# Performance work log

Measured on AMD Instinct MI355X. Metric: run time of the kernel, lower is better.

## Reference

```python
import jax, jax.numpy as jnp
import numpy as np

DIM = 512      # projection dimension
NCOLS = 16384  # number of vectors being projected


def _gram_schmidt(w):
    """Modified Gram-Schmidt, column by column, faithful to the torch loop.

    Columns of q beyond the current index are zero, so the inner loop can
    safely run over all `dim` columns (projections onto zero columns are
    no-ops), which keeps the body shape-static for lax.fori_loop.
    """
    dim = w.shape[1]
    q = jnp.zeros_like(w).at[:, 0].set(w[:, 0] / jnp.linalg.norm(w[:, 0]))

    def outer(i, q):
        v = w[:, i]
        def inner(j, v):
            # modified GS: v is updated sequentially against each prior q_j
            return v - jnp.dot(v, q[:, j]) * q[:, j]
        v = jax.lax.fori_loop(0, dim, inner, v)
        return q.at[:, i].set(v / jnp.linalg.norm(v))

    return jax.lax.fori_loop(1, dim, outer, q)


def setup_inputs() -> dict:
    key = jax.random.key(0)
    k1, k2, k3 = jax.random.split(key, 3)
    return {
        "x": jax.random.normal(k1, (DIM, NCOLS), dtype=jnp.float32),
        "weight": jax.random.normal(k2, (DIM, DIM), dtype=jnp.float32),   # OrthogonalMatrix.weight ~ randn
        "D_param": jax.random.uniform(k3, (DIM,), dtype=jnp.float32),     # ProjectionNetwork.D ~ rand
    }


def reference(x, weight, D_param):
    U = _gram_schmidt(weight)                 # (dim, dim) orthogonal
    D = jax.nn.sigmoid(D_param)               # (dim,)
    P = (U * D[None, :]) @ U.T                # U @ diag(D) @ U^T
    return P @ x                              # (dim, ncols)
```

## Files before the change

### kernel.cpp

```cpp
#include <hip/hip_runtime.h>
#include <hip/hip_bf16.h>

#define DIM 512
#define NCOLS 16384

typedef __bf16 bf16x8 __attribute__((ext_vector_type(8)));
typedef float f32x4 __attribute__((ext_vector_type(4)));

__device__ __forceinline__ unsigned short f2bf(float f) {
  unsigned u = __builtin_bit_cast(unsigned, f);
  u += 0x7FFFu + ((u >> 16) & 1u);
  return (unsigned short)(u >> 16);
}

__global__ __launch_bounds__(256) void k_gram(const float* __restrict__ W,
                                              double* __restrict__ G) {
  __shared__ float Wa[16][34];
  __shared__ float Wb[16][34];
  const int t = threadIdx.x;
  const int tx = t & 15, ty = t >> 4;
  const int i0 = blockIdx.y * 32, j0 = blockIdx.x * 32;
  const int rr = t >> 4, c2 = (t & 15) * 2;
  double acc[2][2] = {{0, 0}, {0, 0}};

  for (int kr = 0; kr < DIM; kr += 16) {
    __syncthreads();
    *(float2*)&Wa[rr][c2] = *(const float2*)&W[(kr + rr) * DIM + i0 + c2];
    *(float2*)&Wb[rr][c2] = *(const float2*)&W[(kr + rr) * DIM + j0 + c2];
    __syncthreads();
#pragma unroll
    for (int r = 0; r < 16; ++r) {
      float2 wi = *(const float2*)&Wa[r][ty * 2];
      float2 wj = *(const float2*)&Wb[r][tx * 2];
      acc[0][0] += (double)wi.x * (double)wj.x;
      acc[0][1] += (double)wi.x * (double)wj.y;
      acc[1][0] += (double)wi.y * (double)wj.x;
      acc[1][1] += (double)wi.y * (double)wj.y;
    }
  }
#pragma unroll
  for (int a = 0; a < 2; ++a)
#pragma unroll
    for (int b = 0; b < 2; ++b)
      G[(i0 + ty * 2 + a) * DIM + j0 + tx * 2 + b] = acc[a][b];
}

__global__ __launch_bounds__(512) void k_panel(double* __restrict__ G,
                                               float* __restrict__ Lf,
                                               int k) {
  __shared__ double A[64][65];
  __shared__ double invd[64];
  const int tid = threadIdx.x;
  const int base = k * 64;

  for (int e = tid; e < 4096; e += 512) {
    int i = e >> 6, j = e & 63;
    A[i][j] = G[(base + i) * DIM + base + j];
  }
  __syncthreads();

#pragma unroll 1
  for (int c = 0; c < 64; ++c) {
    double inv = 1.0 / A[c][c];
#pragma unroll
    for (int q = 0; q < 8; ++q) {
      int e = q * 512 + tid;
      int i = e >> 6, j = e & 63;
      if (j > c && i >= j)
        A[i][j] -= A[i][c] * (A[j][c] * inv);
    }
    __syncthreads();
    double rs = sqrt(inv);
    if (tid == c) invd[c] = rs;
    if (tid < 64 && tid >= c) A[tid][c] *= rs;
  }
  __syncthreads();

  for (int e = tid; e < 4096; e += 512) {
    int i = e >> 6, j = e & 63;
    Lf[(base + i) * DIM + base + j] = (i >= j) ? (float)A[i][j] : 0.f;
  }

  const int r = base + 64 + tid;
  if (r < DIM) {
    double x[64];
#pragma unroll
    for (int j = 0; j < 64; ++j) x[j] = G[r * DIM + base + j];
#pragma unroll
    for (int j = 0; j < 64; ++j) {
      double s0 = 0, s1 = 0, s2 = 0, s3 = 0;
#pragma unroll
      for (int c = 0; c < j; ++c) {
        double t = x[c] * A[j][c];
        if ((c & 3) == 0) s0 += t;
        else if ((c & 3) == 1) s1 += t;
        else if ((c & 3) == 2) s2 += t;
        else s3 += t;
      }
      x[j] = (x[j] - ((s0 + s1) + (s2 + s3))) * invd[j];
    }
#pragma unroll
    for (int j = 0; j < 64; ++j) {
      G[r * DIM + base + j] = x[j];
      Lf[r * DIM + base + j] = (float)x[j];
    }
  }
}

__global__ __launch_bounds__(256) void k_syrk(double* __restrict__ G, int k) {
  __shared__ double Lat[64][34];
  __shared__ double Lbt[64][34];
  const int off = (k + 1) * 64, pb = k * 64;
  const int t = threadIdx.x;
  const int bx = blockIdx.x, by = blockIdx.y;
  if (bx > by) return;
  const int j0 = off + bx * 32, i0 = off + by * 32;
  const int tx = t & 15, ty = t >> 4;

  {
    const int ii = t >> 3, c0 = (t & 7) * 8;
    const double* gi = &G[(i0 + ii) * DIM + pb + c0];
    const double* gj = &G[(j0 + ii) * DIM + pb + c0];
#pragma unroll
    for (int q = 0; q < 4; ++q) {
      double2 va = *(const double2*)(gi + 2 * q);
      double2 vb = *(const double2*)(gj + 2 * q);
      Lat[c0 + 2 * q][ii] = va.x; Lat[c0 + 2 * q + 1][ii] = va.y;
      Lbt[c0 + 2 * q][ii] = vb.x; Lbt[c0 + 2 * q + 1][ii] = vb.y;
    }
  }
  __syncthreads();

  double acc[2][2] = {{0, 0}, {0, 0}};
#pragma unroll 8
  for (int c = 0; c < 64; ++c) {
    double2 la = *(const double2*)&Lat[c][ty * 2];
    double2 lb = *(const double2*)&Lbt[c][tx * 2];
    acc[0][0] += la.x * lb.x; acc[0][1] += la.x * lb.y;
    acc[1][0] += la.y * lb.x; acc[1][1] += la.y * lb.y;
  }
#pragma unroll
  for (int a = 0; a < 2; ++a)
#pragma unroll
    for (int b = 0; b < 2; ++b) {
      int i = i0 + ty * 2 + a, j = j0 + tx * 2 + b;
      G[i * DIM + j] -= acc[a][b];
    }
}

__global__ __launch_bounds__(64) void k_dinv(const float* __restrict__ Lf,
                                             float* __restrict__ Minv) {
  __shared__ float Ld[64][65];
  const int lane = threadIdx.x;
  const int b = blockIdx.x * 64;
  for (int r = 0; r < 64; ++r) Ld[r][lane] = Lf[(b + r) * DIM + b + lane];
  __syncthreads();
  float y[64];
#pragma unroll
  for (int i = 0; i < 64; ++i) {
    float s = (i == lane) ? 1.f : 0.f;
#pragma unroll
    for (int c = 0; c < i; ++c) s -= Ld[i][c] * y[c];
    y[i] = s / Ld[i][i];
  }
  for (int i = 0; i < 64; ++i) Minv[(b + i) * DIM + b + lane] = y[i];
}

__global__ __launch_bounds__(256) void k_combT(const float* __restrict__ Lf,
                                               const float* __restrict__ Minv,
                                               float* __restrict__ T, int n) {
  const int p = blockIdx.z;
  const int rb = p * 2 * n + n, cb = p * 2 * n;
  const int j = blockIdx.x * 16 + (threadIdx.x & 15);
  const int i = blockIdx.y * 16 + (threadIdx.x >> 4);
  float acc = 0.f;
#pragma unroll 4
  for (int c = 0; c < n; ++c)
    acc += Lf[(rb + i) * DIM + cb + c] * Minv[(cb + c) * DIM + cb + j];
  T[p * n * n + i * n + j] = acc;
}

__global__ __launch_bounds__(256) void k_combO(float* __restrict__ Minv,
                                               const float* __restrict__ T, int n) {
  const int p = blockIdx.z;
  const int rb = p * 2 * n + n, cb = p * 2 * n;
  const int j = blockIdx.x * 16 + (threadIdx.x & 15);
  const int i = blockIdx.y * 16 + (threadIdx.x >> 4);
  float acc = 0.f;
#pragma unroll 4
  for (int c = 0; c < n; ++c)
    acc += Minv[(rb + i) * DIM + rb + c] * T[p * n * n + c * n + j];
  Minv[(rb + i) * DIM + cb + j] = -acc;
}

__global__ __launch_bounds__(256) void k_formU(const float* __restrict__ W,
                                               const float* __restrict__ Minv,
                                               float* __restrict__ U) {
  __shared__ float Wt[32][34];
  __shared__ float Mt[32][34];
  const int t = threadIdx.x;
  const int tx = t & 15, ty = t >> 4;
  const int i0 = blockIdx.x * 32, r0 = blockIdx.y * 32;
  const int sr = t >> 3, sc = (t & 7) * 4;
  float acc[2][2] = {{0, 0}, {0, 0}};

  for (int kc = 0; kc < DIM; kc += 32) {
    __syncthreads();
    float4 vw = *(const float4*)&W[(r0 + sr) * DIM + kc + sc];
    float4 vm = *(const float4*)&Minv[(i0 + sr) * DIM + kc + sc];
    Wt[sc + 0][sr] = vw.x; Wt[sc + 1][sr] = vw.y;
    Wt[sc + 2][sr] = vw.z; Wt[sc + 3][sr] = vw.w;
    Mt[sc + 0][sr] = vm.x; Mt[sc + 1][sr] = vm.y;
    Mt[sc + 2][sr] = vm.z; Mt[sc + 3][sr] = vm.w;
    __syncthreads();
#pragma unroll 8
    for (int c = 0; c < 32; ++c) {
      float2 wv = *(const float2*)&Wt[c][ty * 2];
      float2 mv = *(const float2*)&Mt[c][tx * 2];
      acc[0][0] += wv.x * mv.x; acc[0][1] += wv.x * mv.y;
      acc[1][0] += wv.y * mv.x; acc[1][1] += wv.y * mv.y;
    }
  }
#pragma unroll
  for (int a = 0; a < 2; ++a)
#pragma unroll
    for (int b = 0; b < 2; ++b)
      U[(r0 + ty * 2 + a) * DIM + i0 + tx * 2 + b] = acc[a][b];
}

__global__ __launch_bounds__(256) void k_formP(const float* __restrict__ Uin,
                                               const float* __restrict__ Dp,
                                               unsigned short* __restrict__ P) {
  __shared__ float dsh[DIM];
  __shared__ unsigned short As[64][40];
  __shared__ unsigned short Bs[64][40];
  const int t = threadIdx.x;
  const int lane = t & 63, w = t >> 6;
  const int i0 = blockIdx.y * 64, j0 = blockIdx.x * 64;
  const int row = t >> 2, seg = t & 3;

  dsh[t] = 1.f / (1.f + __expf(-Dp[t]));
  dsh[t + 256] = 1.f / (1.f + __expf(-Dp[t + 256]));

  f32x4 acc[4];
#pragma unroll
  for (int nf = 0; nf < 4; ++nf) acc[nf] = (f32x4){0.f, 0.f, 0.f, 0.f};

#pragma unroll 1
  for (int kc = 0; kc < DIM; kc += 32) {
    __syncthreads();
    const int c0 = kc + seg * 8;
    float4 ua = *(const float4*)&Uin[(i0 + row) * DIM + c0];
    float4 ub = *(const float4*)&Uin[(i0 + row) * DIM + c0 + 4];
    float4 va = *(const float4*)&Uin[(j0 + row) * DIM + c0];
    float4 vb = *(const float4*)&Uin[(j0 + row) * DIM + c0 + 4];
    uint4 pa, pb;
    pa.x = (unsigned)f2bf(ua.x * dsh[c0 + 0]) | ((unsigned)f2bf(ua.y * dsh[c0 + 1]) << 16);
    pa.y = (unsigned)f2bf(ua.z * dsh[c0 + 2]) | ((unsigned)f2bf(ua.w * dsh[c0 + 3]) << 16);
    pa.z = (unsigned)f2bf(ub.x * dsh[c0 + 4]) | ((unsigned)f2bf(ub.y * dsh[c0 + 5]) << 16);
    pa.w = (unsigned)f2bf(ub.z * dsh[c0 + 6]) | ((unsigned)f2bf(ub.w * dsh[c0 + 7]) << 16);
    pb.x = (unsigned)f2bf(va.x) | ((unsigned)f2bf(va.y) << 16);
    pb.y = (unsigned)f2bf(va.z) | ((unsigned)f2bf(va.w) << 16);
    pb.z = (unsigned)f2bf(vb.x) | ((unsigned)f2bf(vb.y) << 16);
    pb.w = (unsigned)f2bf(vb.z) | ((unsigned)f2bf(vb.w) << 16);
    *(uint4*)&As[row][seg * 8] = pa;
    *(uint4*)&Bs[row][seg * 8] = pb;
    __syncthreads();
    bf16x8 af = *(const bf16x8*)&As[w * 16 + (lane & 15)][(lane >> 4) * 8];
#pragma unroll
    for (int nf = 0; nf < 4; ++nf) {
      bf16x8 bf = *(const bf16x8*)&Bs[nf * 16 + (lane & 15)][(lane >> 4) * 8];
      acc[nf] = __builtin_amdgcn_mfma_f32_16x16x32_bf16(af, bf, acc[nf], 0, 0, 0);
    }
  }
#pragma unroll
  for (int nf = 0; nf < 4; ++nf)
#pragma unroll
    for (int r = 0; r < 4; ++r) {
      int ri = i0 + w * 16 + (lane >> 4) * 4 + r;
      int cj = j0 + nf * 16 + (lane & 15);
      P[ri * DIM + cj] = f2bf(acc[nf][r]);
    }
}

__global__ __launch_bounds__(512) void k_gemm(const unsigned short* __restrict__ P,
                                              const float* __restrict__ X,
                                              float* __restrict__ out) {
  __shared__ unsigned short As[DIM][40];
  __shared__ unsigned short Bs[64][40];
  const int tid = threadIdx.x;
  const int lane = tid & 63;
  const int w = tid >> 6;
  const int bn = blockIdx.x * 64;
  const int kk = tid >> 4;
  const int nq = tid & 15;

  const unsigned short* prow = P + tid * DIM;
  uint4 a0 = *(const uint4*)(prow + 0);
  uint4 a1 = *(const uint4*)(prow + 8);
  uint4 a2 = *(const uint4*)(prow + 16);
  uint4 a3 = *(const uint4*)(prow + 24);
  float4 bx = *(const float4*)(X + kk * NCOLS + bn + nq * 4);

  f32x4 acc[4][4];
#pragma unroll
  for (int mf = 0; mf < 4; ++mf)
#pragma unroll
    for (int nf = 0; nf < 4; ++nf)
      acc[mf][nf] = (f32x4){0.f, 0.f, 0.f, 0.f};

#pragma unroll 1
  for (int t = 0; t < 16; ++t) {
    __syncthreads();
    *(uint4*)&As[tid][0] = a0;
    *(uint4*)&As[tid][8] = a1;
    *(uint4*)&As[tid][16] = a2;
    *(uint4*)&As[tid][24] = a3;
    Bs[nq * 4 + 0][kk] = f2bf(bx.x);
    Bs[nq * 4 + 1][kk] = f2bf(bx.y);
    Bs[nq * 4 + 2][kk] = f2bf(bx.z);
    Bs[nq * 4 + 3][kk] = f2bf(bx.w);
    if (t < 15) {
      const unsigned short* pn = prow + (t + 1) * 32;
      a0 = *(const uint4*)(pn + 0);
      a1 = *(const uint4*)(pn + 8);
      a2 = *(const uint4*)(pn + 16);
      a3 = *(const uint4*)(pn + 24);
      bx = *(const float4*)(X + ((t + 1) * 32 + kk) * NCOLS + bn + nq * 4);
    }
    __syncthreads();
    bf16x8 af[4], bf[4];
#pragma unroll
    for (int mf = 0; mf < 4; ++mf)
      af[mf] = *(const bf16x8*)&As[w * 64 + mf * 16 + (lane & 15)][(lane >> 4) * 8];
#pragma unroll
    for (int nf = 0; nf < 4; ++nf)
      bf[nf] = *(const bf16x8*)&Bs[nf * 16 + (lane & 15)][(lane >> 4) * 8];
#pragma unroll
    for (int mf = 0; mf < 4; ++mf)
#pragma unroll
      for (int nf = 0; nf < 4; ++nf)
        acc[mf][nf] = __builtin_amdgcn_mfma_f32_16x16x32_bf16(af[mf], bf[nf],
                                                              acc[mf][nf], 0, 0, 0);
  }

#pragma unroll
  for (int mf = 0; mf < 4; ++mf)
#pragma unroll
    for (int nf = 0; nf < 4; ++nf)
#pragma unroll
      for (int r = 0; r < 4; ++r) {
        int row = w * 64 + mf * 16 + (lane >> 4) * 4 + r;
        int col = bn + nf * 16 + (lane & 15);
        out[row * NCOLS + col] = acc[mf][nf][r];
      }
}

extern "C" void kernel_launch(void* const* d_in, const int* in_sizes, int n_in,
                              void* d_out, int out_size, void* d_ws, size_t ws_size,
                              hipStream_t stream) {
  const float* X = (const float*)d_in[0];
  const float* W = (const float*)d_in[1];
  const float* Dp = (const float*)d_in[2];
  float* out = (float*)d_out;

  char* ws = (char*)d_ws;
  double* G = (double*)ws;
  float* Lf = (float*)(ws + (2u << 20));
  float* Minv = (float*)(ws + (3u << 20));
  float* U = (float*)(ws + (4u << 20));
  unsigned short* P = (unsigned short*)(ws + (5u << 20));
  float* T = (float*)ws;

  k_gram<<<dim3(16, 16), 256, 0, stream>>>(W, G);
  hipMemsetAsync(Minv, 0, DIM * DIM * sizeof(float), stream);
  for (int k = 0; k < 8; ++k) {
    k_panel<<<1, 512, 0, stream>>>(G, Lf, k);
    int rem = 7 - k;
    if (rem > 0)
      k_syrk<<<dim3(rem * 2, rem * 2), 256, 0, stream>>>(G, k);
  }
  k_dinv<<<8, 64, 0, stream>>>(Lf, Minv);
  for (int l = 0; l < 3; ++l) {
    int n = 64 << l, Pn = 4 >> l;
    k_combT<<<dim3(n / 16, n / 16, Pn), 256, 0, stream>>>(Lf, Minv, T, n);
    k_combO<<<dim3(n / 16, n / 16, Pn), 256, 0, stream>>>(Minv, T, n);
  }
  k_formU<<<dim3(16, 16), 256, 0, stream>>>(W, Minv, U);
  k_formP<<<dim3(8, 8), 256, 0, stream>>>(U, Dp, P);
  k_gemm<<<NCOLS / 64, 512, 0, stream>>>(P, X, out);
}
```

Baseline: 750.2 us.

## Split Cholesky panel into diagonal factor and multi-block TRSM kernels

The single-block panel kernel is split into a diagonal Cholesky kernel (256 threads, unscaled LDL-style elimination with precomputed reciprocals and scaling applied at write-out) and a separate TRSM kernel launched with one 64-thread block per remaining 64-row block. The triangular solve for the off-diagonal rows is thus spread across several workgroups instead of running on 448 threads of one block. It adds one extra kernel launch per step, and the diagonal elimination is reorganized to cut per-column sync work.

Result: slower. 907.8 us (+21.0%).

```diff
diff --git a/kernel.cpp b/kernel.cpp
--- a/kernel.cpp
+++ b/kernel.cpp
@@ -45,65 +45,80 @@
       G[(i0 + ty * 2 + a) * DIM + j0 + tx * 2 + b] = acc[a][b];
 }
 
-__global__ __launch_bounds__(512) void k_panel(double* __restrict__ G,
-                                               float* __restrict__ Lf,
-                                               int k) {
+__global__ __launch_bounds__(256) void k_diag(double* __restrict__ G,
+                                              float* __restrict__ Lf,
+                                              int k) {
   __shared__ double A[64][65];
-  __shared__ double invd[64];
-  const int tid = threadIdx.x;
+  __shared__ double invL[64];
+  __shared__ double rsL[64];
+  const int t = threadIdx.x;
   const int base = k * 64;
-
-  for (int e = tid; e < 4096; e += 512) {
-    int i = e >> 6, j = e & 63;
-    A[i][j] = G[(base + i) * DIM + base + j];
-  }
+  const int i = t >> 2, g = t & 3;
+
+  for (int e = t; e < 4096; e += 256)
+    A[e >> 6][e & 63] = G[(base + (e >> 6)) * DIM + base + (e & 63)];
+  __syncthreads();
+  if (t == 0) invL[0] = 1.0 / A[0][0];
   __syncthreads();
 
 #pragma unroll 1
   for (int c = 0; c < 64; ++c) {
-    double inv = 1.0 / A[c][c];
-#pragma unroll
-    for (int q = 0; q < 8; ++q) {
-      int e = q * 512 + tid;
-      int i = e >> 6, j = e & 63;
-      if (j > c && i >= j)
-        A[i][j] -= A[i][c] * (A[j][c] * inv);
-    }
-    __syncthreads();
-    double rs = sqrt(inv);
-    if (tid == c) invd[c] = rs;
-    if (tid < 64 && tid >= c) A[tid][c] *= rs;
-  }
-  __syncthreads();
-
-  for (int e = tid; e < 4096; e += 512) {
+    const double inv = invL[c];
+    const double aic = A[i][c];
+    const int j0 = (c + 1) + ((g - (c + 1)) & 3);
+    for (int j = j0; j <= i; j += 4)
+      A[i][j] -= aic * (A[j][c] * inv);
+    if (c < 63 && t == (((c + 1) << 2) | ((c + 1) & 3)))
+      invL[c + 1] = 1.0 / A[c + 1][c + 1];
+    __syncthreads();
+  }
+
+  if (t < 64) rsL[t] = 1.0 / sqrt(A[t][t]);
+  __syncthreads();
+  for (int e = t; e < 4096; e += 256) {
+    int r = e >> 6, j = e & 63;
+    double val = (r >= j) ? A[r][j] * rsL[j] : 0.0;
+    G[(base + r) * DIM + base + j] = val;
+    Lf[(base + r) * DIM + base + j] = (float)val;
+  }
+}
+
+__global__ __launch_bounds__(64, 1) void k_trsm(double* __restrict__ G,
+                                                float* __restrict__ Lf,
+                                                int k) {
+  __shared__ double Ls[64][65];
+  __shared__ double invd[64];
+  const int base = k * 64;
+  const int tid = threadIdx.x;
+  for (int e = tid; e < 4096; e += 64) {
     int i = e >> 6, j = e & 63;
-    Lf[(base + i) * DIM + base + j] = (i >= j) ? (float)A[i][j] : 0.f;
-  }
-
-  const int r = base + 64 + tid;
-  if (r < DIM) {
-    double x[64];
-#pragma unroll
-    for (int j = 0; j < 64; ++j) x[j] = G[r * DIM + base + j];
-#pragma unroll
-    for (int j = 0; j < 64; ++j) {
-      double s0 = 0, s1 = 0, s2 = 0, s3 = 0;
-#pragma unroll
-      for (int c = 0; c < j; ++c) {
-        double t = x[c] * A[j][c];
-        if ((c & 3) == 0) s0 += t;
-        else if ((c & 3) == 1) s1 += t;
-        else if ((c & 3) == 2) s2 += t;
-        else s3 += t;
-      }
-      x[j] = (x[j] - ((s0 + s1) + (s2 + s3))) * invd[j];
-    }
-#pragma unroll
-    for (int j = 0; j < 64; ++j) {
-      G[r * DIM + base + j] = x[j];
-      Lf[r * DIM + base + j] = (float)x[j];
-    }
+    Ls[i][j] = G[(base + i) * DIM + base + j];
+  }
+  __syncthreads();
+  invd[tid] = 1.0 / Ls[tid][tid];
+  __syncthreads();
+
+  const int r = base + 64 + blockIdx.x * 64 + tid;
+  double x[64];
+#pragma unroll
+  for (int j = 0; j < 64; ++j) x[j] = G[r * DIM + base + j];
+#pragma unroll
+  for (int j = 0; j < 64; ++j) {
+    double s0 = 0, s1 = 0, s2 = 0, s3 = 0;
+#pragma unroll
+    for (int c = 0; c < j; ++c) {
+      double tt = x[c] * Ls[j][c];
+      if ((c & 3) == 0) s0 += tt;
+      else if ((c & 3) == 1) s1 += tt;
+      else if ((c & 3) == 2) s2 += tt;
+      else s3 += tt;
+    }
+    x[j] = (x[j] - ((s0 + s1) + (s2 + s3))) * invd[j];
+  }
+#pragma unroll
+  for (int j = 0; j < 64; ++j) {
+    G[r * DIM + base + j] = x[j];
+    Lf[r * DIM + base + j] = (float)x[j];
   }
 }
 
@@ -143,8 +158,8 @@
   for (int a = 0; a < 2; ++a)
 #pragma unroll
     for (int b = 0; b < 2; ++b) {
-      int i = i0 + ty * 2 + a, j = j0 + tx * 2 + b;
-      G[i * DIM + j] -= acc[a][b];
+      int ii = i0 + ty * 2 + a, jj = j0 + tx * 2 + b;
+      G[ii * DIM + jj] -= acc[a][b];
     }
 }
 
@@ -375,10 +390,12 @@
   k_gram<<<dim3(16, 16), 256, 0, stream>>>(W, G);
   hipMemsetAsync(Minv, 0, DIM * DIM * sizeof(float), stream);
   for (int k = 0; k < 8; ++k) {
-    k_panel<<<1, 512, 0, stream>>>(G, Lf, k);
+    k_diag<<<1, 256, 0, stream>>>(G, Lf, k);
     int rem = 7 - k;
-    if (rem > 0)
+    if (rem > 0) {
+      k_trsm<<<rem, 64, 0, stream>>>(G, Lf, k);
       k_syrk<<<dim3(rem * 2, rem * 2), 256, 0, stream>>>(G, k);
+    }
   }
   k_dinv<<<8, 64, 0, stream>>>(Lf, Minv);
   for (int l = 0; l < 3; ++l) {
```
